# Optimization experiments

Hardware: AMD Instinct MI355X
Metric: run time of the kernel (lower is better)

Reference implementation:

```python
import jax, jax.numpy as jnp
import numpy as np
from jax import lax

DN = ('NCHW', 'OIHW', 'NCHW')

def conv(x, w, pad='VALID'):
    return lax.conv_general_dilated(x, w, (1, 1), pad, dimension_numbers=DN)

def adaptive_matrix(in_s, out_s):
    # exact torch adaptive_avg_pool2d bin weights: start=floor(i*in/out), end=ceil((i+1)*in/out)
    M = np.zeros((out_s, in_s), np.float32)
    for i in range(out_s):
        s = (i * in_s) // out_s
        e = -(-((i + 1) * in_s) // out_s)
        M[i, s:e] = 1.0 / (e - s)
    return jnp.asarray(M)

def setup_inputs() -> dict:
    key = jax.random.key(0)
    ks = jax.random.split(key, 11)
    C = 64
    def w(k, shape, fan_in):
        return jax.random.normal(k, shape, jnp.float32) * (1.0 / np.sqrt(fan_in))
    return {
        'x': jax.random.normal(ks[0], (16, C, 128, 128), jnp.float32),
        'conv1_w': w(ks[1], (2 * C, C, 1, 1), C),
        'conv1_b': jnp.zeros((2 * C,), jnp.float32),
        'conv2_w': w(ks[2], (C, C, 1, 1), C),
        'conv2_b': jnp.zeros((C,), jnp.float32),
        'conv3_w': w(ks[3], (C, 2 * C, 1, 1), 2 * C),
        'conv3_b': jnp.zeros((C,), jnp.float32),
        'pos_w': w(ks[4], (C, C, 3, 3), C * 9),
        'pos_b': jnp.zeros((C,), jnp.float32),
        'se_w1': w(ks[5], (C // 8, C, 1, 1), C),
        'se_w2': w(ks[6], (C, C // 8, 1, 1), C // 8),
    }

def reference(x, conv1_w, conv1_b, conv2_w, conv2_b, conv3_w, conv3_b, pos_w, pos_b, se_w1, se_w2):
    C, nw, ext = 64, 4, 4
    y = conv(x, conv1_w) + conv1_b[None, :, None, None]
    x1, x2 = y[:, :C], y[:, C:]
    N, _, H, W = x1.shape
    x1p = jnp.pad(x1, ((0, 0), (0, 0), (ext, ext), (ext, ext)), mode='edge')
    Hp, Wp = H + 2 * ext, W + 2 * ext
    Hs, Ws = H // nw, W // nw
    Hk, Wk = Hs + H % nw, Ws + W % nw
    Hps, Wps = Hp // nw, Wp // nw
    Hpk, Wpk = Hps + Hp % nw, Wps + Wp % nw
    # unfold: windows row-major (h_window fastest over j), shape (N, nw^2, C, Hpk, Wpk)
    wins = jnp.stack([x1p[:, :, i * Hps:i * Hps + Hpk, j * Wps:j * Wps + Wpk]
                      for i in range(nw) for j in range(nw)], axis=1)
    Ph = adaptive_matrix(Hpk, Hk)
    Pw = adaptive_matrix(Wpk, Wk)
    pooled = jnp.einsum('nlchw,Hh,Ww->nlcHW', wins, Ph, Pw).reshape(N * nw * nw, C, Hk, Wk)
    pr = (conv(pooled, conv2_w) + conv2_b[None, :, None, None]
          + conv(pooled, pos_w, 'SAME') + pos_b[None, :, None, None])
    # SE attention
    s = jnp.mean(pr, axis=(2, 3), keepdims=True)
    s = jax.nn.sigmoid(conv(jax.nn.relu(conv(s, se_w1)), se_w2))
    att = pr * s + pr
    # faithful torch .view(N, C*Hk*Wk, nw^2) memory reinterpretation, then fold
    cols = att.reshape(N, nw * nw * C * Hk * Wk).reshape(N, C, Hk, Wk, nw * nw)
    out = jnp.zeros((N, C, H, W), x.dtype)
    cnt = jnp.zeros((N, 1, H, W), x.dtype)
    for i in range(nw):
        for j in range(nw):
            l = i * nw + j
            out = out.at[:, :, i * Hs:i * Hs + Hk, j * Ws:j * Ws + Wk].add(cols[..., l])
            cnt = cnt.at[:, :, i * Hs:i * Hs + Hk, j * Ws:j * Ws + Wk].add(1.0)
    out = out / cnt
    return conv(jnp.concatenate([out, x2], axis=1), conv3_w) + conv3_b[None, :, None, None]
```

## Files before the change

kernel.cpp:

```cpp
#include <hip/hip_runtime.h>

constexpr int N = 16, C = 64, H = 128, W = 128, P = H * W;
constexpr int NL = 256, PK = 1024;

constexpr size_t OFF_RA    = 0;
constexpr size_t OFF_RB    = 8388608;
constexpr size_t OFF_RC    = 16777216;
constexpr size_t OFF_SUMS  = 25165824;
constexpr size_t OFF_SCALE = OFF_SUMS  + 16384;
constexpr size_t OFF_WMOD  = OFF_SCALE + 16384;
constexpr size_t OFF_W1L   = OFF_WMOD  + 18432;
constexpr size_t OFF_W3L   = OFF_W1L   + 4096;

typedef short bf16x8 __attribute__((ext_vector_type(8)));
typedef float f32x4  __attribute__((ext_vector_type(4)));

__device__ inline unsigned short f2bf(float f) {
    unsigned u = __float_as_uint(f);
    unsigned r = (u + 0x7FFFu + ((u >> 16) & 1u)) >> 16;
    return (unsigned short)r;
}
__device__ inline float bf2f(unsigned short h) {
    return __uint_as_float(((unsigned)h) << 16);
}

__global__ __launch_bounds__(256) void k0_prep(const float* __restrict__ pos_w,
                                               const float* __restrict__ conv2_w,
                                               const float* __restrict__ w1,
                                               const float* __restrict__ w3,
                                               unsigned short* __restrict__ wmod,
                                               unsigned short* __restrict__ w1lay,
                                               unsigned short* __restrict__ w3lay,
                                               float* __restrict__ sums) {
    int t = blockIdx.x * 256 + threadIdx.x;
    if (t < 36864) {
        int cir = t & 31;
        int co  = (t >> 5) & 63;
        int cib = (t >> 11) & 1;
        int tap = t >> 12;
        int ci  = cib * 32 + cir;
        float v = pos_w[(co * 64 + ci) * 9 + tap];
        if (tap == 4) v += conv2_w[co * 64 + ci];
        wmod[t] = f2bf(v);
    } else if (t < 45056) {
        int u = t - 36864;
        int cir = u & 31;
        int co  = (u >> 5) & 127;
        int cib = u >> 12;
        w1lay[u] = f2bf(w1[co * 64 + cib * 32 + cir]);
    } else if (t < 53248) {
        int u = t - 45056;
        int cir = u & 31;
        int co  = (u >> 5) & 63;
        int cib = u >> 11;
        w3lay[u] = f2bf(w3[co * 128 + cib * 32 + cir]);
    } else {
        sums[t - 53248] = 0.f;
    }
}

__global__ __launch_bounds__(256) void k1_conv1(const float* __restrict__ x,
                                                const unsigned short* __restrict__ w1lay,
                                                const float* __restrict__ b1,
                                                unsigned short* __restrict__ x1t,
                                                unsigned short* __restrict__ x2t) {
    int bid = blockIdx.x;
    int n   = bid >> 7;
    int px0 = (bid & 127) << 7;
    int t   = threadIdx.x;
    int wave = t >> 6, lane = t & 63;
    int quad = lane >> 4, l16 = lane & 15;
    int pxw = wave * 32;
    const float* xb = x + (size_t)n * 64 * P + px0 + pxw + l16;
    bf16x8 bfr[2][2];
    #pragma unroll
    for (int cib = 0; cib < 2; ++cib) {
        #pragma unroll
        for (int pt = 0; pt < 2; ++pt) {
            unsigned short tmp[8];
            #pragma unroll
            for (int q = 0; q < 8; ++q)
                tmp[q] = f2bf(xb[(size_t)(cib * 32 + quad * 8 + q) * P + pt * 16]);
            bfr[cib][pt] = *(const bf16x8*)tmp;
        }
    }
    f32x4 acc[8][2] = {};
    #pragma unroll
    for (int cib = 0; cib < 2; ++cib) {
        bf16x8 af[8];
        #pragma unroll
        for (int ct = 0; ct < 8; ++ct)
            af[ct] = *(const bf16x8*)(w1lay + ((size_t)(cib * 128 + ct * 16 + l16)) * 32 + quad * 8);
        #pragma unroll
        for (int ct = 0; ct < 8; ++ct)
            #pragma unroll
            for (int pt = 0; pt < 2; ++pt)
                acc[ct][pt] = __builtin_amdgcn_mfma_f32_16x16x32_bf16(af[ct], bfr[cib][pt], acc[ct][pt], 0, 0, 0);
    }
    #pragma unroll
    for (int ct = 0; ct < 8; ++ct) {
        int co0 = ct * 16 + quad * 4;
        float4 bb = *(const float4*)(b1 + co0);
        #pragma unroll
        for (int pt = 0; pt < 2; ++pt) {
            int px = px0 + pxw + pt * 16 + l16;
            ushort4 o;
            o.x = f2bf(acc[ct][pt][0] + bb.x);
            o.y = f2bf(acc[ct][pt][1] + bb.y);
            o.z = f2bf(acc[ct][pt][2] + bb.z);
            o.w = f2bf(acc[ct][pt][3] + bb.w);
            if (co0 < 64)
                *(ushort4*)(x1t + ((size_t)n * P + px) * 64 + co0) = o;
            else
                *(ushort4*)(x2t + ((size_t)n * P + px) * 64 + (co0 - 64)) = o;
        }
    }
}

__global__ __launch_bounds__(256) void k3_pool_pr(const unsigned short* __restrict__ x1t,
                                                  const unsigned short* __restrict__ wmod,
                                                  const float* __restrict__ b2,
                                                  const float* __restrict__ posb,
                                                  unsigned short* __restrict__ prb,
                                                  float* __restrict__ sums) {
    __shared__ __align__(16) unsigned short lxs[340 * 32];
    __shared__ __align__(16) unsigned short lwm[9 * 64 * 32];
    int bid = blockIdx.x;
    int nl  = bid >> 2;
    int r0  = (bid & 3) * 8;
    int n   = nl >> 4, wl = nl & 15;
    int wi  = wl >> 2, wj = wl & 3;
    int t   = threadIdx.x;
    const unsigned short* xb = x1t + (size_t)n * P * 64;
    int wave = t >> 6, lane = t & 63;
    int quad = lane >> 4, l16 = lane & 15;
    int wrow0 = wave * 2;
    f32x4 acc[4][4] = {};
    #pragma unroll
    for (int cib = 0; cib < 2; ++cib) {
        if (cib) __syncthreads();
        for (int it = 0; it < 6; ++it) {
            int e = t + it * 256;
            if (e < 1360) {
                int pix = e >> 2, part = e & 3;
                int lr = pix / 34, lc = pix - lr * 34;
                int gr = r0 - 1 + lr, gc = lc - 1;
                unsigned short oc[8];
                if ((unsigned)gr < 32u && (unsigned)gc < 32u) {
                    int sh = gr + (gr >> 4), sw = gc + (gc >> 4);
                    int u = wi * 34 + sh - 4, v = wj * 34 + sw - 4;
                    int ra = min(max(u, 0), 127), rb = min(max(u + 1, 0), 127);
                    int ca = min(max(v, 0), 127), cb = min(max(v + 1, 0), 127);
                    int off = cib * 32 + part * 8;
                    uint4 A = *(const uint4*)(xb + (size_t)(ra * 128 + ca) * 64 + off);
                    uint4 B = *(const uint4*)(xb + (size_t)(ra * 128 + cb) * 64 + off);
                    uint4 Cc = *(const uint4*)(xb + (size_t)(rb * 128 + ca) * 64 + off);
                    uint4 D = *(const uint4*)(xb + (size_t)(rb * 128 + cb) * 64 + off);
                    const unsigned short* a = (const unsigned short*)&A;
                    const unsigned short* b = (const unsigned short*)&B;
                    const unsigned short* c = (const unsigned short*)&Cc;
                    const unsigned short* d = (const unsigned short*)&D;
                    #pragma unroll
                    for (int q = 0; q < 8; ++q)
                        oc[q] = f2bf(0.25f * (bf2f(a[q]) + bf2f(b[q]) + bf2f(c[q]) + bf2f(d[q])));
                } else {
                    #pragma unroll
                    for (int q = 0; q < 8; ++q) oc[q] = 0;
                }
                *(uint4*)(lxs + pix * 32 + ((part ^ ((pix >> 1) & 3)) * 8)) = *(const uint4*)oc;
            }
        }
        #pragma unroll
        for (int it = 0; it < 9; ++it) {
            int e = t + it * 256;
            int tap = e >> 8, rem = e & 255;
            int co = rem >> 2, part = rem & 3;
            *(uint4*)(lwm + (tap * 64 + co) * 32 + ((part ^ ((co >> 1) & 3)) * 8)) =
                *(const uint4*)(wmod + (((size_t)(tap * 2 + cib) * 64 + co) * 32) + part * 8);
        }
        __syncthreads();
        #pragma unroll
        for (int tap = 0; tap < 9; ++tap) {
            int dh = tap / 3, dw = tap % 3;
            bf16x8 af[4], bfr[4];
            #pragma unroll
            for (int ct = 0; ct < 4; ++ct) {
                int co = ct * 16 + l16;
                af[ct] = *(const bf16x8*)(lwm + (tap * 64 + co) * 32 + ((quad ^ ((co >> 1) & 3)) * 8));
            }
            #pragma unroll
            for (int pt = 0; pt < 4; ++pt) {
                int pix = (wrow0 + (pt >> 1) + dh) * 34 + ((pt & 1) * 16 + l16 + dw);
                bfr[pt] = *(const bf16x8*)(lxs + pix * 32 + ((quad ^ ((pix >> 1) & 3)) * 8));
            }
            #pragma unroll
            for (int ct = 0; ct < 4; ++ct)
                #pragma unroll
                for (int pt = 0; pt < 4; ++pt)
                    acc[ct][pt] = __builtin_amdgcn_mfma_f32_16x16x32_bf16(af[ct], bfr[pt], acc[ct][pt], 0, 0, 0);
        }
    }
    #pragma unroll
    for (int ct = 0; ct < 4; ++ct) {
        #pragma unroll
        for (int r = 0; r < 4; ++r) {
            int co = ct * 16 + quad * 4 + r;
            float bias = b2[co] + posb[co];
            float s = 0.f;
            #pragma unroll
            for (int pt = 0; pt < 4; ++pt) {
                float v = acc[ct][pt][r] + bias;
                int row = r0 + wrow0 + (pt >> 1);
                int col = (pt & 1) * 16 + l16;
                prb[(size_t)nl * 65536 + co * 1024 + row * 32 + col] = f2bf(v);
                s += v;
            }
            s += __shfl_xor(s, 1);
            s += __shfl_xor(s, 2);
            s += __shfl_xor(s, 4);
            s += __shfl_xor(s, 8);
            if (l16 == 0) atomicAdd(&sums[nl * 64 + co], s);
        }
    }
}

__global__ __launch_bounds__(256) void k3b_se(const float* __restrict__ sums,
                                              const float* __restrict__ w1,
                                              const float* __restrict__ w2,
                                              float* __restrict__ scale) {
    int wv   = (blockIdx.x << 2) + (threadIdx.x >> 6);
    int lane = threadIdx.x & 63;
    float m = sums[wv * 64 + lane] * (1.f / 1024.f);
    int h = lane >> 3, sub = lane & 7;
    float p = 0.f;
    #pragma unroll
    for (int k = 0; k < 8; ++k) {
        int ci = sub * 8 + k;
        p += w1[h * 64 + ci] * __shfl(m, ci);
    }
    p += __shfl_xor(p, 1);
    p += __shfl_xor(p, 2);
    p += __shfl_xor(p, 4);
    float hid = fmaxf(p, 0.f);
    float v = 0.f;
    #pragma unroll
    for (int r = 0; r < 8; ++r)
        v += w2[lane * 8 + r] * __shfl(hid, r * 8);
    scale[wv * 64 + lane] = 1.f + 1.f / (1.f + __expf(-v));
}

__global__ __launch_bounds__(256) void k5_conv3(const unsigned short* __restrict__ prb,
                                                const float* __restrict__ scale,
                                                const unsigned short* __restrict__ x2t,
                                                const unsigned short* __restrict__ w3lay,
                                                const float* __restrict__ b3,
                                                float* __restrict__ out) {
    __shared__ __align__(16) unsigned short lxs[128 * 136];
    int bid = blockIdx.x;
    int n   = bid >> 7;
    int row = bid & 127;
    int i   = row >> 5, h2 = row & 31;
    int px0 = row << 7;
    int t   = threadIdx.x;
    const unsigned short* src2 = x2t + ((size_t)n * P + (size_t)row * 128) * 64;
    #pragma unroll
    for (int it = 0; it < 4; ++it) {
        int e = t + it * 256;
        int pix = e >> 3, part = e & 7;
        *(uint4*)(lxs + pix * 136 + 64 + part * 8) = *(const uint4*)(src2 + pix * 64 + part * 8);
    }
    int c2 = t >> 5, w2 = t & 31;
    int cc_b = h2 >> 1;
    int hb = (h2 & 1) * 512 + w2 * 16 + i * 4;
    #pragma unroll
    for (int mm = 0; mm < 2; ++mm) {
        int nl = n * 16 + c2 * 2 + mm;
        const unsigned short* pb = prb + (size_t)nl * 65536 + (size_t)cc_b * 1024 + hb;
        const float* sb = scale + nl * 64 + cc_b;
        ushort4 v0 = *(const ushort4*)(pb);
        ushort4 v1 = *(const ushort4*)(pb + 16 * 1024);
        ushort4 v2 = *(const ushort4*)(pb + 32 * 1024);
        ushort4 v3 = *(const ushort4*)(pb + 48 * 1024);
        float s0 = sb[0], s1 = sb[16], s2 = sb[32], s3 = sb[48];
        unsigned short* d = lxs + w2 * 136 + c2 * 8 + mm * 4;
        ushort4 o;
        o.x = f2bf(bf2f(v0.x) * s0); o.y = f2bf(bf2f(v1.x) * s1);
        o.z = f2bf(bf2f(v2.x) * s2); o.w = f2bf(bf2f(v3.x) * s3);
        *(ushort4*)(d) = o;
        o.x = f2bf(bf2f(v0.y) * s0); o.y = f2bf(bf2f(v1.y) * s1);
        o.z = f2bf(bf2f(v2.y) * s2); o.w = f2bf(bf2f(v3.y) * s3);
        *(ushort4*)(d + 32 * 136) = o;
        o.x = f2bf(bf2f(v0.z) * s0); o.y = f2bf(bf2f(v1.z) * s1);
        o.z = f2bf(bf2f(v2.z) * s2); o.w = f2bf(bf2f(v3.z) * s3);
        *(ushort4*)(d + 64 * 136) = o;
        o.x = f2bf(bf2f(v0.w) * s0); o.y = f2bf(bf2f(v1.w) * s1);
        o.z = f2bf(bf2f(v2.w) * s2); o.w = f2bf(bf2f(v3.w) * s3);
        *(ushort4*)(d + 96 * 136) = o;
    }
    __syncthreads();
    int wave = t >> 6, lane = t & 63;
    int quad = lane >> 4, l16 = lane & 15;
    int pxw = wave * 32;
    f32x4 acc[4][2] = {};
    #pragma unroll
    for (int cib = 0; cib < 4; ++cib) {
        bf16x8 af[4], bfr[2];
        #pragma unroll
        for (int ct = 0; ct < 4; ++ct)
            af[ct] = *(const bf16x8*)(w3lay + ((size_t)(cib * 64 + ct * 16 + l16)) * 32 + quad * 8);
        #pragma unroll
        for (int pt = 0; pt < 2; ++pt)
            bfr[pt] = *(const bf16x8*)(lxs + (pxw + pt * 16 + l16) * 136 + cib * 32 + quad * 8);
        #pragma unroll
        for (int ct = 0; ct < 4; ++ct)
            #pragma unroll
            for (int pt = 0; pt < 2; ++pt)
                acc[ct][pt] = __builtin_amdgcn_mfma_f32_16x16x32_bf16(af[ct], bfr[pt], acc[ct][pt], 0, 0, 0);
    }
    #pragma unroll
    for (int ct = 0; ct < 4; ++ct) {
        int co0 = ct * 16 + quad * 4;
        float4 bb = *(const float4*)(b3 + co0);
        #pragma unroll
        for (int pt = 0; pt < 2; ++pt) {
            int px = px0 + pxw + pt * 16 + l16;
            const float* bp = (const float*)&bb;
            #pragma unroll
            for (int r = 0; r < 4; ++r)
                out[((size_t)n * 64 + co0 + r) * P + px] = acc[ct][pt][r] + bp[r];
        }
    }
}

extern "C" void kernel_launch(void* const* d_in, const int* in_sizes, int n_in,
                              void* d_out, int out_size, void* d_ws, size_t ws_size,
                              hipStream_t stream) {
    const float* x       = (const float*)d_in[0];
    const float* conv1_w = (const float*)d_in[1];
    const float* conv1_b = (const float*)d_in[2];
    const float* conv2_w = (const float*)d_in[3];
    const float* conv2_b = (const float*)d_in[4];
    const float* conv3_w = (const float*)d_in[5];
    const float* conv3_b = (const float*)d_in[6];
    const float* pos_w   = (const float*)d_in[7];
    const float* pos_b   = (const float*)d_in[8];
    const float* se_w1   = (const float*)d_in[9];
    const float* se_w2   = (const float*)d_in[10];

    float* ws = (float*)d_ws;
    unsigned short* prb  = (unsigned short*)(ws + OFF_RA);
    unsigned short* x1t  = (unsigned short*)(ws + OFF_RB);
    unsigned short* x2t  = (unsigned short*)(ws + OFF_RC);
    float* sums  = ws + OFF_SUMS;
    float* scale = ws + OFF_SCALE;
    unsigned short* wmod  = (unsigned short*)(ws + OFF_WMOD);
    unsigned short* w1lay = (unsigned short*)(ws + OFF_W1L);
    unsigned short* w3lay = (unsigned short*)(ws + OFF_W3L);

    k0_prep   <<<272,  256, 0, stream>>>(pos_w, conv2_w, conv1_w, conv3_w,
                                         wmod, w1lay, w3lay, sums);
    k1_conv1  <<<2048, 256, 0, stream>>>(x, w1lay, conv1_b, x1t, x2t);
    k3_pool_pr<<<1024, 256, 0, stream>>>(x1t, wmod, conv2_b, pos_b, prb, sums);
    k3b_se    <<<64,   256, 0, stream>>>(sums, se_w1, se_w2, scale);
    k5_conv3  <<<2048, 256, 0, stream>>>(prb, scale, x2t, w3lay, conv3_b, (float*)d_out);
}
```

Measured before the change: 226.3 us.

## Fold conv1 x2 branch into conv3 weights and drop x2 intermediate

```diff
diff --git a/kernel.cpp b/kernel.cpp
--- a/kernel.cpp
+++ b/kernel.cpp
@@ -5,12 +5,12 @@
 
 constexpr size_t OFF_RA    = 0;
 constexpr size_t OFF_RB    = 8388608;
-constexpr size_t OFF_RC    = 16777216;
-constexpr size_t OFF_SUMS  = 25165824;
+constexpr size_t OFF_SUMS  = 16777216;
 constexpr size_t OFF_SCALE = OFF_SUMS  + 16384;
 constexpr size_t OFF_WMOD  = OFF_SCALE + 16384;
 constexpr size_t OFF_W1L   = OFF_WMOD  + 18432;
 constexpr size_t OFF_W3L   = OFF_W1L   + 4096;
+constexpr size_t OFF_B3F   = OFF_W3L   + 4096;
 
 typedef short bf16x8 __attribute__((ext_vector_type(8)));
 typedef float f32x4  __attribute__((ext_vector_type(4)));
@@ -28,10 +28,13 @@
                                                const float* __restrict__ conv2_w,
                                                const float* __restrict__ w1,
                                                const float* __restrict__ w3,
+                                               const float* __restrict__ b1,
+                                               const float* __restrict__ b3,
                                                unsigned short* __restrict__ wmod,
                                                unsigned short* __restrict__ w1lay,
                                                unsigned short* __restrict__ w3lay,
-                                               float* __restrict__ sums) {
+                                               float* __restrict__ sums,
+                                               float* __restrict__ b3f) {
     int t = blockIdx.x * 256 + threadIdx.x;
     if (t < 36864) {
         int cir = t & 31;
@@ -53,17 +56,33 @@
         int cir = u & 31;
         int co  = (u >> 5) & 63;
         int cib = u >> 11;
-        w3lay[u] = f2bf(w3[co * 128 + cib * 32 + cir]);
-    } else {
+        float v;
+        if (cib < 2) {
+            v = w3[co * 128 + cib * 32 + cir];
+        } else {
+            int ci = (cib - 2) * 32 + cir;
+            v = 0.f;
+            #pragma unroll
+            for (int k = 0; k < 64; ++k)
+                v += w3[co * 128 + 64 + k] * w1[(64 + k) * 64 + ci];
+        }
+        w3lay[u] = f2bf(v);
+    } else if (t < 69632) {
         sums[t - 53248] = 0.f;
+    } else if (t < 69696) {
+        int co = t - 69632;
+        float s = b3[co];
+        #pragma unroll
+        for (int k = 0; k < 64; ++k)
+            s += w3[co * 128 + 64 + k] * b1[64 + k];
+        b3f[co] = s;
     }
 }
 
 __global__ __launch_bounds__(256) void k1_conv1(const float* __restrict__ x,
                                                 const unsigned short* __restrict__ w1lay,
                                                 const float* __restrict__ b1,
-                                                unsigned short* __restrict__ x1t,
-                                                unsigned short* __restrict__ x2t) {
+                                                unsigned short* __restrict__ x1t) {
     int bid = blockIdx.x;
     int n   = bid >> 7;
     int px0 = (bid & 127) << 7;
@@ -84,21 +103,21 @@
             bfr[cib][pt] = *(const bf16x8*)tmp;
         }
     }
-    f32x4 acc[8][2] = {};
+    f32x4 acc[4][2] = {};
     #pragma unroll
     for (int cib = 0; cib < 2; ++cib) {
-        bf16x8 af[8];
-        #pragma unroll
-        for (int ct = 0; ct < 8; ++ct)
+        bf16x8 af[4];
+        #pragma unroll
+        for (int ct = 0; ct < 4; ++ct)
             af[ct] = *(const bf16x8*)(w1lay + ((size_t)(cib * 128 + ct * 16 + l16)) * 32 + quad * 8);
         #pragma unroll
-        for (int ct = 0; ct < 8; ++ct)
+        for (int ct = 0; ct < 4; ++ct)
             #pragma unroll
             for (int pt = 0; pt < 2; ++pt)
                 acc[ct][pt] = __builtin_amdgcn_mfma_f32_16x16x32_bf16(af[ct], bfr[cib][pt], acc[ct][pt], 0, 0, 0);
     }
     #pragma unroll
-    for (int ct = 0; ct < 8; ++ct) {
+    for (int ct = 0; ct < 4; ++ct) {
         int co0 = ct * 16 + quad * 4;
         float4 bb = *(const float4*)(b1 + co0);
         #pragma unroll
@@ -109,10 +128,7 @@
             o.y = f2bf(acc[ct][pt][1] + bb.y);
             o.z = f2bf(acc[ct][pt][2] + bb.z);
             o.w = f2bf(acc[ct][pt][3] + bb.w);
-            if (co0 < 64)
-                *(ushort4*)(x1t + ((size_t)n * P + px) * 64 + co0) = o;
-            else
-                *(ushort4*)(x2t + ((size_t)n * P + px) * 64 + (co0 - 64)) = o;
+            *(ushort4*)(x1t + ((size_t)n * P + px) * 64 + co0) = o;
         }
     }
 }
@@ -124,7 +140,6 @@
                                                   unsigned short* __restrict__ prb,
                                                   float* __restrict__ sums) {
     __shared__ __align__(16) unsigned short lxs[340 * 32];
-    __shared__ __align__(16) unsigned short lwm[9 * 64 * 32];
     int bid = blockIdx.x;
     int nl  = bid >> 2;
     int r0  = (bid & 3) * 8;
@@ -170,24 +185,14 @@
                 *(uint4*)(lxs + pix * 32 + ((part ^ ((pix >> 1) & 3)) * 8)) = *(const uint4*)oc;
             }
         }
-        #pragma unroll
-        for (int it = 0; it < 9; ++it) {
-            int e = t + it * 256;
-            int tap = e >> 8, rem = e & 255;
-            int co = rem >> 2, part = rem & 3;
-            *(uint4*)(lwm + (tap * 64 + co) * 32 + ((part ^ ((co >> 1) & 3)) * 8)) =
-                *(const uint4*)(wmod + (((size_t)(tap * 2 + cib) * 64 + co) * 32) + part * 8);
-        }
         __syncthreads();
         #pragma unroll
         for (int tap = 0; tap < 9; ++tap) {
             int dh = tap / 3, dw = tap % 3;
             bf16x8 af[4], bfr[4];
             #pragma unroll
-            for (int ct = 0; ct < 4; ++ct) {
-                int co = ct * 16 + l16;
-                af[ct] = *(const bf16x8*)(lwm + (tap * 64 + co) * 32 + ((quad ^ ((co >> 1) & 3)) * 8));
-            }
+            for (int ct = 0; ct < 4; ++ct)
+                af[ct] = *(const bf16x8*)(wmod + (((tap * 2 + cib) * 64) + ct * 16 + l16) * 32 + quad * 8);
             #pragma unroll
             for (int pt = 0; pt < 4; ++pt) {
                 int pix = (wrow0 + (pt >> 1) + dh) * 34 + ((pt & 1) * 16 + l16 + dw);
@@ -251,23 +256,32 @@
 
 __global__ __launch_bounds__(256) void k5_conv3(const unsigned short* __restrict__ prb,
                                                 const float* __restrict__ scale,
-                                                const unsigned short* __restrict__ x2t,
+                                                const float* __restrict__ x,
                                                 const unsigned short* __restrict__ w3lay,
-                                                const float* __restrict__ b3,
+                                                const float* __restrict__ b3f,
                                                 float* __restrict__ out) {
-    __shared__ __align__(16) unsigned short lxs[128 * 136];
+    __shared__ __align__(16) unsigned short lxs[128 * 72];
     int bid = blockIdx.x;
     int n   = bid >> 7;
     int row = bid & 127;
     int i   = row >> 5, h2 = row & 31;
     int px0 = row << 7;
     int t   = threadIdx.x;
-    const unsigned short* src2 = x2t + ((size_t)n * P + (size_t)row * 128) * 64;
-    #pragma unroll
-    for (int it = 0; it < 4; ++it) {
-        int e = t + it * 256;
-        int pix = e >> 3, part = e & 7;
-        *(uint4*)(lxs + pix * 136 + 64 + part * 8) = *(const uint4*)(src2 + pix * 64 + part * 8);
+    int wave = t >> 6, lane = t & 63;
+    int quad = lane >> 4, l16 = lane & 15;
+    int pxw = wave * 32;
+    const float* xb = x + (size_t)n * 64 * P + px0 + pxw + l16;
+    bf16x8 bx[2][2];
+    #pragma unroll
+    for (int cib = 0; cib < 2; ++cib) {
+        #pragma unroll
+        for (int pt = 0; pt < 2; ++pt) {
+            unsigned short tmp[8];
+            #pragma unroll
+            for (int q = 0; q < 8; ++q)
+                tmp[q] = f2bf(xb[(size_t)(cib * 32 + quad * 8 + q) * P + pt * 16]);
+            bx[cib][pt] = *(const bf16x8*)tmp;
+        }
     }
     int c2 = t >> 5, w2 = t & 31;
     int cc_b = h2 >> 1;
@@ -282,25 +296,22 @@
         ushort4 v2 = *(const ushort4*)(pb + 32 * 1024);
         ushort4 v3 = *(const ushort4*)(pb + 48 * 1024);
         float s0 = sb[0], s1 = sb[16], s2 = sb[32], s3 = sb[48];
-        unsigned short* d = lxs + w2 * 136 + c2 * 8 + mm * 4;
+        unsigned short* d = lxs + w2 * 72 + c2 * 8 + mm * 4;
         ushort4 o;
         o.x = f2bf(bf2f(v0.x) * s0); o.y = f2bf(bf2f(v1.x) * s1);
         o.z = f2bf(bf2f(v2.x) * s2); o.w = f2bf(bf2f(v3.x) * s3);
         *(ushort4*)(d) = o;
         o.x = f2bf(bf2f(v0.y) * s0); o.y = f2bf(bf2f(v1.y) * s1);
         o.z = f2bf(bf2f(v2.y) * s2); o.w = f2bf(bf2f(v3.y) * s3);
-        *(ushort4*)(d + 32 * 136) = o;
+        *(ushort4*)(d + 32 * 72) = o;
         o.x = f2bf(bf2f(v0.z) * s0); o.y = f2bf(bf2f(v1.z) * s1);
         o.z = f2bf(bf2f(v2.z) * s2); o.w = f2bf(bf2f(v3.z) * s3);
-        *(ushort4*)(d + 64 * 136) = o;
+        *(ushort4*)(d + 64 * 72) = o;
         o.x = f2bf(bf2f(v0.w) * s0); o.y = f2bf(bf2f(v1.w) * s1);
         o.z = f2bf(bf2f(v2.w) * s2); o.w = f2bf(bf2f(v3.w) * s3);
-        *(ushort4*)(d + 96 * 136) = o;
+        *(ushort4*)(d + 96 * 72) = o;
     }
     __syncthreads();
-    int wave = t >> 6, lane = t & 63;
-    int quad = lane >> 4, l16 = lane & 15;
-    int pxw = wave * 32;
     f32x4 acc[4][2] = {};
     #pragma unroll
     for (int cib = 0; cib < 4; ++cib) {
@@ -309,8 +320,12 @@
         for (int ct = 0; ct < 4; ++ct)
             af[ct] = *(const bf16x8*)(w3lay + ((size_t)(cib * 64 + ct * 16 + l16)) * 32 + quad * 8);
         #pragma unroll
-        for (int pt = 0; pt < 2; ++pt)
-            bfr[pt] = *(const bf16x8*)(lxs + (pxw + pt * 16 + l16) * 136 + cib * 32 + quad * 8);
+        for (int pt = 0; pt < 2; ++pt) {
+            if (cib < 2)
+                bfr[pt] = *(const bf16x8*)(lxs + (pxw + pt * 16 + l16) * 72 + cib * 32 + quad * 8);
+            else
+                bfr[pt] = bx[cib - 2][pt];
+        }
         #pragma unroll
         for (int ct = 0; ct < 4; ++ct)
             #pragma unroll
@@ -320,7 +335,7 @@
     #pragma unroll
     for (int ct = 0; ct < 4; ++ct) {
         int co0 = ct * 16 + quad * 4;
-        float4 bb = *(const float4*)(b3 + co0);
+        float4 bb = *(const float4*)(b3f + co0);
         #pragma unroll
         for (int pt = 0; pt < 2; ++pt) {
             int px = px0 + pxw + pt * 16 + l16;
@@ -350,17 +365,18 @@
     float* ws = (float*)d_ws;
     unsigned short* prb  = (unsigned short*)(ws + OFF_RA);
     unsigned short* x1t  = (unsigned short*)(ws + OFF_RB);
-    unsigned short* x2t  = (unsigned short*)(ws + OFF_RC);
     float* sums  = ws + OFF_SUMS;
     float* scale = ws + OFF_SCALE;
     unsigned short* wmod  = (unsigned short*)(ws + OFF_WMOD);
     unsigned short* w1lay = (unsigned short*)(ws + OFF_W1L);
     unsigned short* w3lay = (unsigned short*)(ws + OFF_W3L);
-
-    k0_prep   <<<272,  256, 0, stream>>>(pos_w, conv2_w, conv1_w, conv3_w,
-                                         wmod, w1lay, w3lay, sums);
-    k1_conv1  <<<2048, 256, 0, stream>>>(x, w1lay, conv1_b, x1t, x2t);
+    float* b3f   = ws + OFF_B3F;
+
+    k0_prep   <<<273,  256, 0, stream>>>(pos_w, conv2_w, conv1_w, conv3_w,
+                                         conv1_b, conv3_b,
+                                         wmod, w1lay, w3lay, sums, b3f);
+    k1_conv1  <<<2048, 256, 0, stream>>>(x, w1lay, conv1_b, x1t);
     k3_pool_pr<<<1024, 256, 0, stream>>>(x1t, wmod, conv2_b, pos_b, prb, sums);
     k3b_se    <<<64,   256, 0, stream>>>(sums, se_w1, se_w2, scale);
-    k5_conv3  <<<2048, 256, 0, stream>>>(prb, scale, x2t, w3lay, conv3_b, (float*)d_out);
-}
+    k5_conv3  <<<2048, 256, 0, stream>>>(prb, scale, x, w3lay, b3f, (float*)d_out);
+}
```

Result: faster. 217.5 us (-3.9%).
